# Optimization experiments

Measured on AMD Instinct MI355X. Metric: run time of the kernel, lower is better.

The kernel has to match this reference:

```python
import jax, jax.numpy as jnp
import numpy as np

# ---- static config (from init_kwargs / hard-coded DMlp structure) ----
B, H, W = 8, 56, 56
C = 576              # dim = 9 * n_feat
NF = 64              # n_feat (channels after PixelShuffle(3))
NH = 6               # num_heads
WS = 7               # window_size
N = H * W
IN_F, HID_F, OUT_F = NF * 25, NF * 16, NF * 9  # DMlp fc dims (1600, 1024, 576)

# the hard-coded 7x7 selection mask in DMlp (25 True positions of 49)
_MASK = np.array([
    [1,0,0,1,0,0,1],
    [0,1,0,1,0,1,0],
    [0,0,1,1,1,0,0],
    [1,1,1,1,1,1,1],
    [0,0,1,1,1,0,0],
    [0,1,0,1,0,1,0],
    [1,0,0,1,0,0,1]], dtype=bool)
_OFFS = [(int(i), int(j)) for i, j in np.argwhere(_MASK)]  # row-major, matches masked_select order


def _rel_pos_index(ws):
    coords = np.stack(np.meshgrid(np.arange(ws), np.arange(ws), indexing='ij'))  # (2, ws, ws)
    cf = coords.reshape(2, -1)
    rel = (cf[:, :, None] - cf[:, None, :]).transpose(1, 2, 0).astype(np.int64)
    rel[..., 0] += ws - 1
    rel[..., 1] += ws - 1
    rel[..., 0] *= 2 * ws - 1
    return rel.sum(-1)  # (ws*ws, ws*ws)

REL_IDX = jnp.asarray(_rel_pos_index(WS))


def layernorm(x, w, b, eps=1e-5):
    mu = x.mean(-1, keepdims=True)
    var = ((x - mu) ** 2).mean(-1, keepdims=True)
    return (x - mu) / jnp.sqrt(var + eps) * w + b


def dmlp(x, fc1_w, fc1_b, fc2_w, fc2_b):
    # x: (B, N, C). Patch_UnEmbed(patch_dim=1) == reshape to (B, C, H, W)
    y = x.transpose(0, 2, 1).reshape(B, C, H, W)
    # PixelShuffle(3): (B, C, H, W) -> (B, NF, 3H, 3W)
    y = y.reshape(B, NF, 3, 3, H, W).transpose(0, 1, 4, 2, 5, 3).reshape(B, NF, 3 * H, 3 * W)
    # ReflectionPad2d(2)
    y = jnp.pad(y, ((0, 0), (0, 0), (2, 2), (2, 2)), mode='reflect')
    # unfold(kernel=7, stride=3) + masked_select: gather only the 25 masked kernel offsets
    cols = jnp.stack([y[:, :, di:di + 3 * H:3, dj:dj + 3 * W:3] for di, dj in _OFFS], axis=-1)  # (B, NF, H, W, 25)
    cols = cols.transpose(0, 2, 3, 1, 4).reshape(B, N, IN_F)  # channel-major then kernel pos, like masked_select
    h = jax.nn.gelu(cols @ fc1_w + fc1_b, approximate=False)
    return h @ fc2_w + fc2_b  # (B, N, OUT_F=C)


def reference(x, norm1_w, norm1_b, qkv_w, qkv_b, rpb_table, proj_w, proj_b,
              norm2_w, norm2_b, fc1_w, fc1_b, fc2_w, fc2_b):
    shortcut = x
    y = layernorm(x, norm1_w, norm1_b).reshape(B, H, W, C)
    # window partition (shift_size = 0, no mask)
    nw = H // WS
    yw = y.reshape(B, nw, WS, nw, WS, C).transpose(0, 1, 3, 2, 4, 5).reshape(-1, WS * WS, C)
    # window attention with relative position bias
    qkv = yw @ qkv_w + qkv_b  # (B*nW^2, 49, 3C)
    hd = C // NH
    q, k, v = [t.reshape(-1, WS * WS, NH, hd).transpose(0, 2, 1, 3) for t in jnp.split(qkv, 3, axis=-1)]
    scale = hd ** -0.5
    attn = jnp.einsum('bhid,bhjd->bhij', q * scale, k)
    bias = rpb_table[REL_IDX].transpose(2, 0, 1)  # (NH, 49, 49)
    attn = jax.nn.softmax(attn + bias[None], axis=-1)
    o = jnp.einsum('bhij,bhjd->bhid', attn, v).transpose(0, 2, 1, 3).reshape(-1, WS * WS, C)
    o = o @ proj_w + proj_b
    # window reverse
    o = o.reshape(B, nw, nw, WS, WS, C).transpose(0, 1, 3, 2, 4, 5).reshape(B, N, C)
    x = shortcut + o
    x = x + dmlp(layernorm(x, norm2_w, norm2_b), fc1_w, fc1_b, fc2_w, fc2_b)
    return x


def setup_inputs() -> dict:
    key = jax.random.key(0)
    ks = jax.random.split(key, 16)
    s = 0.02
    return {
        'x': jax.random.normal(ks[0], (B, N, C), jnp.float32),
        'norm1_w': jnp.ones((C,), jnp.float32),
        'norm1_b': jnp.zeros((C,), jnp.float32),
        'qkv_w': jax.random.normal(ks[1], (C, 3 * C), jnp.float32) * s,
        'qkv_b': jnp.zeros((3 * C,), jnp.float32),
        'rpb_table': jax.random.normal(ks[2], ((2 * WS - 1) ** 2, NH), jnp.float32) * s,
        'proj_w': jax.random.normal(ks[3], (C, C), jnp.float32) * s,
        'proj_b': jnp.zeros((C,), jnp.float32),
        'norm2_w': jnp.ones((C,), jnp.float32),
        'norm2_b': jnp.zeros((C,), jnp.float32),
        'fc1_w': jax.random.normal(ks[4], (IN_F, HID_F), jnp.float32) * s,
        'fc1_b': jnp.zeros((HID_F,), jnp.float32),
        'fc2_w': jax.random.normal(ks[5], (HID_F, OUT_F), jnp.float32) * s,
        'fc2_b': jnp.zeros((OUT_F,), jnp.float32),
    }
```

## Files before the change

kernel.cpp:

```cpp
#include <hip/hip_runtime.h>

typedef unsigned short u16;
typedef __bf16 bf16x8 __attribute__((ext_vector_type(8)));
typedef float f32x4 __attribute__((ext_vector_type(4)));

__device__ __forceinline__ float bf2f(u16 u) {
  union { unsigned int i; float f; } v; v.i = ((unsigned int)u) << 16; return v.f;
}
__device__ __forceinline__ u16 f2bf(float f) {
  union { float f; unsigned int i; } v; v.f = f;
  unsigned int i = v.i;
  return (u16)((i + 0x7fffu + ((i >> 16) & 1u)) >> 16);
}
__device__ __forceinline__ float ldf(const float* p) { return *p; }
__device__ __forceinline__ float ldf(const u16* p) { return bf2f(*p); }

__device__ __forceinline__ float gelu_f(float v) {
  float x = fabsf(v) * 0.70710678118654752f;
  float t = __builtin_amdgcn_rcpf(fmaf(0.3275911f, x, 1.0f));
  float poly = t * fmaf(t, fmaf(t, fmaf(t, fmaf(t, 1.061405429f, -1.453152027f),
                                        1.421413741f), -0.284496736f), 0.254829592f);
  float er = fmaf(-poly, __expf(-x * x), 1.0f);
  er = copysignf(er, v);
  return 0.5f * v * (1.0f + er);
}

__device__ __forceinline__ void load_lds16(const u16* g, u16* l) {
  __builtin_amdgcn_global_load_lds(
      (const __attribute__((address_space(1))) unsigned int*)g,
      (__attribute__((address_space(3))) unsigned int*)l, 16, 0, 0);
}

__global__ void transpose_kernel(const float* __restrict__ W, u16* __restrict__ Wt,
                                 int K, int N) {
  int idx = blockIdx.x * 256 + threadIdx.x;
  if (idx >= K * N) return;
  int k = idx / N, n = idx % N;
  Wt[n * K + k] = f2bf(W[idx]);
}

__global__ void transpose_fc1_kernel(const float* __restrict__ W, u16* __restrict__ Wt) {
  int idx = blockIdx.x * 256 + threadIdx.x;
  if (idx >= 1600 * 1024) return;
  int k = idx >> 10, n = idx & 1023;
  int nf = k / 25, p = k - nf * 25;
  Wt[n * 1600 + p * 64 + nf] = f2bf(W[idx]);
}

template <typename T>
__global__ __launch_bounds__(256) void ln_kernel(const T* __restrict__ x,
                                                 const float* __restrict__ w,
                                                 const float* __restrict__ b,
                                                 u16* __restrict__ out) {
  int wave = threadIdx.x >> 6, lane = threadIdx.x & 63;
  long row = (long)blockIdx.x * 4 + wave;
  const T* xr = x + row * 576;
  float v[9];
  float sum = 0.f;
  #pragma unroll
  for (int i = 0; i < 9; ++i) { v[i] = ldf(&xr[lane + i * 64]); sum += v[i]; }
  #pragma unroll
  for (int off = 32; off; off >>= 1) sum += __shfl_xor(sum, off);
  float mean = sum * (1.0f / 576.0f);
  float var = 0.f;
  #pragma unroll
  for (int i = 0; i < 9; ++i) { float d = v[i] - mean; var += d * d; }
  #pragma unroll
  for (int off = 32; off; off >>= 1) var += __shfl_xor(var, off);
  float rstd = rsqrtf(var * (1.0f / 576.0f) + 1e-5f);
  u16* outr = out + row * 576;
  #pragma unroll
  for (int i = 0; i < 9; ++i) {
    int c = lane + i * 64;
    outr[c] = f2bf((v[i] - mean) * rstd * w[c] + b[c]);
  }
}

__global__ __launch_bounds__(256) void ln_ps_kernel(const float* __restrict__ x,
                                                    const float* __restrict__ w,
                                                    const float* __restrict__ b,
                                                    u16* __restrict__ ps) {
  __shared__ u16 sh[4][576];
  int wave = threadIdx.x >> 6, lane = threadIdx.x & 63;
  long row = (long)blockIdx.x * 4 + wave;
  const float* xr = x + row * 576;
  float v[9];
  float sum = 0.f;
  #pragma unroll
  for (int i = 0; i < 9; ++i) { v[i] = xr[lane + i * 64]; sum += v[i]; }
  #pragma unroll
  for (int off = 32; off; off >>= 1) sum += __shfl_xor(sum, off);
  float mean = sum * (1.0f / 576.0f);
  float var = 0.f;
  #pragma unroll
  for (int i = 0; i < 9; ++i) { float d = v[i] - mean; var += d * d; }
  #pragma unroll
  for (int off = 32; off; off >>= 1) var += __shfl_xor(var, off);
  float rstd = rsqrtf(var * (1.0f / 576.0f) + 1e-5f);
  #pragma unroll
  for (int i = 0; i < 9; ++i) {
    int c = lane + i * 64;
    sh[wave][c] = f2bf((v[i] - mean) * rstd * w[c] + b[c]);
  }
  __syncthreads();
  int bb = (int)(row / 3136), ij = (int)(row % 3136);
  int h2 = ij / 56, w2 = ij - h2 * 56;
  #pragma unroll
  for (int a = 0; a < 3; ++a)
    #pragma unroll
    for (int b2 = 0; b2 < 3; ++b2) {
      u16 val = sh[wave][lane * 9 + a * 3 + b2];
      long off = (((long)bb * 168 + 3 * h2 + a) * 168 + (3 * w2 + b2)) * 64 + lane;
      ps[off] = val;
    }
}

__constant__ int c_di[25] = {0,0,0, 1,1,1, 2,2,2, 3,3,3,3,3,3,3, 4,4,4, 5,5,5, 6,6,6};
__constant__ int c_dj[25] = {0,3,6, 1,3,5, 2,3,4, 0,1,2,3,4,5,6, 2,3,4, 1,3,5, 0,3,6};

__global__ __launch_bounds__(256) void attn_kernel(const u16* __restrict__ qkv,
                                                   const float* __restrict__ rpb,
                                                   u16* __restrict__ obuf) {
  int h = blockIdx.y;
  int wi = blockIdx.x;
  int b = wi >> 6, w = wi & 63, wr = w >> 3, wc = w & 7;
  __shared__ __align__(16) u16 Qs[64 * 104];
  __shared__ __align__(16) u16 Ks[64 * 104];
  __shared__ __align__(16) u16 Vt[96 * 72];
  __shared__ __align__(16) u16 Ps[64 * 72];
  int tid = threadIdx.x;
  int lane = tid & 63, wv = tid >> 6;
  int quad = lane >> 4, l15 = lane & 15;
  const float scale = 0.1020620726159658f;

  long base = ((long)b * 3136 + wr * 7 * 56 + wc * 7) * 1728 + h * 96;

  for (int idx = tid; idx < 588; idx += 256) {
    int t = idx / 12, dq = idx % 12;
    int tr = t / 7, tc = t - tr * 7;
    long roff = base + (tr * 56 + tc) * 1728 + dq * 8;
    *(uint4*)&Qs[t * 104 + dq * 8] = *(const uint4*)(qkv + roff);
    *(uint4*)&Ks[t * 104 + dq * 8] = *(const uint4*)(qkv + roff + 576);
  }
  for (int idx = tid; idx < 96 * 15; idx += 256) {
    int d = idx / 15, t = 49 + idx % 15;
    Vt[d * 72 + t] = 0;
  }
  for (int idx = tid; idx < 768; idx += 256) {
    int dq = idx >> 6, t = idx & 63;
    if (t < 49) {
      int tr = t / 7, tc = t - tr * 7;
      uint4 v = *(const uint4*)(qkv + base + (tr * 56 + tc) * 1728 + 1152 + dq * 8);
      const u16* vv = (const u16*)&v;
      #pragma unroll
      for (int kk = 0; kk < 8; ++kk) Vt[(dq * 8 + kk) * 72 + t] = vv[kk];
    }
  }
  __syncthreads();

  f32x4 accS[4] = {};
  #pragma unroll
  for (int k0 = 0; k0 < 3; ++k0) {
    bf16x8 aq = *(const bf16x8*)&Qs[(wv * 16 + l15) * 104 + k0 * 32 + quad * 8];
    #pragma unroll
    for (int nt = 0; nt < 4; ++nt) {
      bf16x8 bk = *(const bf16x8*)&Ks[(nt * 16 + l15) * 104 + k0 * 32 + quad * 8];
      accS[nt] = __builtin_amdgcn_mfma_f32_16x16x32_bf16(aq, bk, accS[nt], 0, 0, 0);
    }
  }

  #pragma unroll
  for (int r = 0; r < 4; ++r) {
    int rg = wv * 16 + quad * 4 + r;
    int yi = rg / 7, xi = rg - yi * 7;
    float sv[4];
    float mx = -3e38f;
    #pragma unroll
    for (int nt = 0; nt < 4; ++nt) {
      int col = nt * 16 + l15;
      float s = accS[nt][r] * scale;
      if (rg < 49 && col < 49) {
        int yj = col / 7, xj = col - yj * 7;
        s += rpb[((yi - yj + 6) * 13 + (xi - xj + 6)) * 6 + h];
      } else {
        s = -3e38f;
      }
      sv[nt] = s;
      mx = fmaxf(mx, s);
    }
    #pragma unroll
    for (int off = 8; off; off >>= 1) mx = fmaxf(mx, __shfl_xor(mx, off));
    float sum = 0.f;
    #pragma unroll
    for (int nt = 0; nt < 4; ++nt) { sv[nt] = __expf(sv[nt] - mx); sum += sv[nt]; }
    #pragma unroll
    for (int off = 8; off; off >>= 1) sum += __shfl_xor(sum, off);
    float inv = 1.0f / sum;
    u16* psr = Ps + rg * 72;
    #pragma unroll
    for (int nt = 0; nt < 4; ++nt) psr[nt * 16 + l15] = f2bf(sv[nt] * inv);
  }
  __syncthreads();

  f32x4 accO[6] = {};
  #pragma unroll
  for (int k0 = 0; k0 < 2; ++k0) {
    bf16x8 ap = *(const bf16x8*)&Ps[(wv * 16 + l15) * 72 + k0 * 32 + quad * 8];
    #pragma unroll
    for (int nt = 0; nt < 6; ++nt) {
      bf16x8 bv = *(const bf16x8*)&Vt[(nt * 16 + l15) * 72 + k0 * 32 + quad * 8];
      accO[nt] = __builtin_amdgcn_mfma_f32_16x16x32_bf16(ap, bv, accO[nt], 0, 0, 0);
    }
  }
  #pragma unroll
  for (int r = 0; r < 4; ++r) {
    int rg = wv * 16 + quad * 4 + r;
    if (rg < 49) {
      int tr = rg / 7, tc = rg - tr * 7;
      long ooff = ((long)b * 3136 + (wr * 7 + tr) * 56 + wc * 7 + tc) * 576 + h * 96;
      #pragma unroll
      for (int nt = 0; nt < 6; ++nt) obuf[ooff + nt * 16 + l15] = f2bf(accO[nt][r]);
    }
  }
}

template <int EPI, typename TR, typename TO>
__global__ __launch_bounds__(256) void gemm_kernel(const u16* __restrict__ A,
                                                   const u16* __restrict__ Bt,
                                                   const float* __restrict__ bias,
                                                   const TR* __restrict__ res,
                                                   TO* __restrict__ C,
                                                   int M, int N, int K) {
  __shared__ __align__(16) u16 As[3][128 * 32];
  __shared__ __align__(16) u16 Bs[3][128 * 32];

  int nwg = gridDim.x * gridDim.y;
  int flat = blockIdx.y * gridDim.x + blockIdx.x;
  int q = nwg >> 3, r = nwg & 7;
  int xcd = flat & 7, loc = flat >> 3;
  int newflat = ((xcd < r) ? xcd * (q + 1) : r * (q + 1) + (xcd - r) * q) + loc;
  int nblk = newflat % gridDim.x, mblk = newflat / gridDim.x;
  int n0 = nblk * 128;
  int m0 = mblk * 128;

  int tid = threadIdx.x;
  int lane = tid & 63, wv = tid >> 6;
  int quad = lane >> 4, l15 = lane & 15;
  int wr2 = wv >> 1, wc2 = wv & 1;
  f32x4 acc[4][4] = {};

  int rA0 = tid >> 2, rA1 = 64 + (tid >> 2);
  int kc0 = (tid & 3) * 8;
  int rB0 = n0 + rA0; if (rB0 > N - 1) rB0 = N - 1;
  int rB1 = n0 + rA1; if (rB1 > N - 1) rB1 = N - 1;
  const u16* gA0 = A + (long)(m0 + rA0) * K + kc0;
  const u16* gA1 = A + (long)(m0 + rA1) * K + kc0;
  const u16* gB0 = Bt + (long)rB0 * K + kc0;
  const u16* gB1 = Bt + (long)rB1 * K + kc0;
  int lo0 = (wv * 64) * 8, lo1 = (256 + wv * 64) * 8;

  int nt = K >> 5;
  auto stage = [&](int bufi, int kk) {
    load_lds16(gA0 + kk, &As[bufi][lo0]);
    load_lds16(gA1 + kk, &As[bufi][lo1]);
    load_lds16(gB0 + kk, &Bs[bufi][lo0]);
    load_lds16(gB1 + kk, &Bs[bufi][lo1]);
  };
  auto compute = [&](int cur) {
    bf16x8 a[4], bfr[4];
    const u16* as = &As[cur][(wr2 * 64 + l15) * 32 + quad * 8];
    const u16* bs = &Bs[cur][(wc2 * 64 + l15) * 32 + quad * 8];
    #pragma unroll
    for (int mi = 0; mi < 4; ++mi) a[mi] = *(const bf16x8*)(as + mi * 512);
    #pragma unroll
    for (int ni = 0; ni < 4; ++ni) bfr[ni] = *(const bf16x8*)(bs + ni * 512);
    #pragma unroll
    for (int mi = 0; mi < 4; ++mi)
      #pragma unroll
      for (int ni = 0; ni < 4; ++ni)
        acc[mi][ni] = __builtin_amdgcn_mfma_f32_16x16x32_bf16(a[mi], bfr[ni], acc[mi][ni], 0, 0, 0);
  };

  stage(0, 0);
  stage(1, 32);
  int cur = 0, nx2 = 2;
  for (int t = 0; t < nt; ++t) {
    if (t + 2 < nt) {
      stage(nx2, (t + 2) * 32);
      asm volatile("s_waitcnt vmcnt(8)" ::: "memory");
    } else if (t + 1 < nt) {
      asm volatile("s_waitcnt vmcnt(4)" ::: "memory");
    } else {
      asm volatile("s_waitcnt vmcnt(0)" ::: "memory");
    }
    __builtin_amdgcn_s_barrier();
    compute(cur);
    __builtin_amdgcn_s_barrier();
    cur = cur + 1; if (cur == 3) cur = 0;
    nx2 = nx2 + 1; if (nx2 == 3) nx2 = 0;
  }

  #pragma unroll
  for (int mi = 0; mi < 4; ++mi)
    #pragma unroll
    for (int ni = 0; ni < 4; ++ni) {
      int col = n0 + wc2 * 64 + ni * 16 + l15;
      if (col < N) {
        float bz = bias[col];
        #pragma unroll
        for (int rr = 0; rr < 4; ++rr) {
          int row = m0 + wr2 * 64 + mi * 16 + quad * 4 + rr;
          float v = acc[mi][ni][rr] + bz;
          if (EPI == 1) v = gelu_f(v);
          if (EPI == 2) v += ldf(&res[(long)row * N + col]);
          long off = (long)row * N + col;
          if (sizeof(TO) == 2) ((u16*)C)[off] = f2bf(v);
          else                 ((float*)C)[off] = v;
        }
      }
    }
}

__global__ __launch_bounds__(256) void fc1_kernel(const u16* __restrict__ ps,
                                                  const u16* __restrict__ Bt,
                                                  const float* __restrict__ bias,
                                                  u16* __restrict__ C) {
  const int N = 1024, K = 1600;
  __shared__ __align__(16) u16 As[2][128 * 32];
  __shared__ __align__(16) u16 Bs[2][128 * 32];
  __shared__ int s_di[25], s_dj[25];
  if (threadIdx.x < 25) {
    s_di[threadIdx.x] = c_di[threadIdx.x];
    s_dj[threadIdx.x] = c_dj[threadIdx.x];
  }

  int nwg = gridDim.x * gridDim.y;
  int flat = blockIdx.y * gridDim.x + blockIdx.x;
  int q = nwg >> 3;
  int xcd = flat & 7, loc = flat >> 3;
  int newflat = xcd * q + loc;
  int nblk = newflat % gridDim.x, mblk = newflat / gridDim.x;
  int n0 = nblk * 128;
  int m0 = mblk * 128;

  int tid = threadIdx.x;
  int lane = tid & 63, wv = tid >> 6;
  int quad = lane >> 4, l15 = lane & 15;
  int wr2 = wv >> 1, wc2 = wv & 1;
  f32x4 acc[4][4] = {};

  int rA0 = tid >> 2, rA1 = 64 + (tid >> 2);
  int kc0 = (tid & 3) * 8;
  int m0_ = m0 + rA0;
  int b0 = m0_ / 3136, ij0 = m0_ % 3136, i0 = ij0 / 56, j0 = ij0 - i0 * 56;
  int m1_ = m0 + rA1;
  int b1 = m1_ / 3136, ij1 = m1_ % 3136, i1 = ij1 / 56, j1 = ij1 - i1 * 56;
  int u0 = 3 * i0 - 2, v0 = 3 * j0 - 2;
  int u1 = 3 * i1 - 2, v1 = 3 * j1 - 2;
  const u16* psb0 = ps + (long)b0 * 1806336 + kc0;
  const u16* psb1 = ps + (long)b1 * 1806336 + kc0;
  const u16* gB0 = Bt + (long)(n0 + rA0) * K + kc0;
  const u16* gB1 = Bt + (long)(n0 + rA1) * K + kc0;
  int lo0 = (wv * 64) * 8, lo1 = (256 + wv * 64) * 8;

  __syncthreads();

  auto stage = [&](int bufi, int t) {
    int p = t >> 1;
    int dip = s_di[p], djp = s_dj[p];
    int nf = (t & 1) << 5;
    int R0 = u0 + dip; R0 = R0 < 0 ? -R0 : R0; R0 = R0 >= 168 ? 334 - R0 : R0;
    int C0 = v0 + djp; C0 = C0 < 0 ? -C0 : C0; C0 = C0 >= 168 ? 334 - C0 : C0;
    int R1 = u1 + dip; R1 = R1 < 0 ? -R1 : R1; R1 = R1 >= 168 ? 334 - R1 : R1;
    int C1 = v1 + djp; C1 = C1 < 0 ? -C1 : C1; C1 = C1 >= 168 ? 334 - C1 : C1;
    load_lds16(psb0 + (((R0 * 168 + C0) << 6) + nf), &As[bufi][lo0]);
    load_lds16(psb1 + (((R1 * 168 + C1) << 6) + nf), &As[bufi][lo1]);
    load_lds16(gB0 + t * 32, &Bs[bufi][lo0]);
    load_lds16(gB1 + t * 32, &Bs[bufi][lo1]);
  };
  auto compute = [&](int cur) {
    bf16x8 a[4], bfr[4];
    const u16* as = &As[cur][(wr2 * 64 + l15) * 32 + quad * 8];
    const u16* bs = &Bs[cur][(wc2 * 64 + l15) * 32 + quad * 8];
    #pragma unroll
    for (int mi = 0; mi < 4; ++mi) a[mi] = *(const bf16x8*)(as + mi * 512);
    #pragma unroll
    for (int ni = 0; ni < 4; ++ni) bfr[ni] = *(const bf16x8*)(bs + ni * 512);
    #pragma unroll
    for (int mi = 0; mi < 4; ++mi)
      #pragma unroll
      for (int ni = 0; ni < 4; ++ni)
        acc[mi][ni] = __builtin_amdgcn_mfma_f32_16x16x32_bf16(a[mi], bfr[ni], acc[mi][ni], 0, 0, 0);
  };

  const int nt = K >> 5;
  stage(0, 0);
  #pragma unroll 2
  for (int t = 0; t < nt - 1; ++t) {
    int cur = t & 1;
    stage(cur ^ 1, t + 1);
    asm volatile("s_waitcnt vmcnt(4)" ::: "memory");
    __builtin_amdgcn_s_barrier();
    compute(cur);
    __builtin_amdgcn_s_barrier();
  }
  asm volatile("s_waitcnt vmcnt(0)" ::: "memory");
  __builtin_amdgcn_s_barrier();
  compute((nt - 1) & 1);

  #pragma unroll
  for (int mi = 0; mi < 4; ++mi)
    #pragma unroll
    for (int ni = 0; ni < 4; ++ni) {
      int col = n0 + wc2 * 64 + ni * 16 + l15;
      float bz = bias[col];
      #pragma unroll
      for (int rr = 0; rr < 4; ++rr) {
        int row = m0 + wr2 * 64 + mi * 16 + quad * 4 + rr;
        C[(long)row * N + col] = f2bf(gelu_f(acc[mi][ni][rr] + bz));
      }
    }
}

extern "C" void kernel_launch(void* const* d_in, const int* in_sizes, int n_in,
                              void* d_out, int out_size, void* d_ws, size_t ws_size,
                              hipStream_t stream) {
  const float* x      = (const float*)d_in[0];
  const float* n1w    = (const float*)d_in[1];
  const float* n1b    = (const float*)d_in[2];
  const float* qkv_w  = (const float*)d_in[3];
  const float* qkv_b  = (const float*)d_in[4];
  const float* rpb    = (const float*)d_in[5];
  const float* proj_w = (const float*)d_in[6];
  const float* proj_b = (const float*)d_in[7];
  const float* n2w    = (const float*)d_in[8];
  const float* n2b    = (const float*)d_in[9];
  const float* fc1_w  = (const float*)d_in[10];
  const float* fc1_b  = (const float*)d_in[11];
  const float* fc2_w  = (const float*)d_in[12];
  const float* fc2_b  = (const float*)d_in[13];

  char* ws = (char*)d_ws;
  u16* wt_qkv  = (u16*)(ws + 0);
  u16* wt_proj = (u16*)(ws + 1990656);
  u16* wt_fc1  = (u16*)(ws + 2654208);
  u16* wt_fc2  = (u16*)(ws + 5931008);
  char* qkvpool = ws + 7110656;
  char* lnpool  = ws + 50462720;
  u16* ln2ps = (u16*)(ws + 7110656);
  u16* hb    = (u16*)(ws + 36012032);
  float* x1 = (float*)d_out;

  transpose_kernel<<<3888, 256, 0, stream>>>(qkv_w, wt_qkv, 576, 1728);
  transpose_kernel<<<1296, 256, 0, stream>>>(proj_w, wt_proj, 576, 576);
  transpose_fc1_kernel<<<6400, 256, 0, stream>>>(fc1_w, wt_fc1);
  transpose_kernel<<<2304, 256, 0, stream>>>(fc2_w, wt_fc2, 1024, 576);

  for (int h = 0; h < 2; ++h) {
    const long r0 = (long)h * 12544;
    u16* lnb  = (u16*)lnpool;
    u16* qkvb = (u16*)qkvpool;
    ln_kernel<float><<<3136, 256, 0, stream>>>(x + r0 * 576, n1w, n1b, lnb);
    gemm_kernel<0, float, u16><<<dim3(14, 98), 256, 0, stream>>>(
        lnb, wt_qkv, qkv_b, (const float*)nullptr, qkvb, 12544, 1728, 576);
    attn_kernel<<<dim3(256, 6), 256, 0, stream>>>(qkvb, rpb, lnb);
    gemm_kernel<2, float, float><<<dim3(5, 98), 256, 0, stream>>>(
        lnb, wt_proj, proj_b, x + r0 * 576, x1 + r0 * 576, 12544, 576, 576);
  }

  ln_ps_kernel<<<6272, 256, 0, stream>>>(x1, n2w, n2b, ln2ps);
  fc1_kernel<<<dim3(8, 196), 256, 0, stream>>>(ln2ps, wt_fc1, fc1_b, hb);
  gemm_kernel<2, float, float><<<dim3(5, 196), 256, 0, stream>>>(
      hb, wt_fc2, fc2_b, x1, x1, 25088, 576, 1024);
}
```

Before: 534.5 us.

## Widen GEMM K-tile to 64 with XOR-swizzled LDS layout, double buffering

Both the generic GEMM and the fused-unfold fc1 kernel now stage a 64-wide K slice per iteration instead of 32. Each 16-byte chunk is placed in LDS with an XOR swizzle so fragment reads avoid bank conflicts. The generic GEMM drops from triple to double buffering. The change aims to halve the barrier and loop overhead per MFMA and cut LDS conflicts, and in fc1 one K-tile now covers a whole kernel offset (all 64 channels). The cost is more LDS per block (64 KB), which may lower occupancy, and shallower prefetch in the generic GEMM.

```diff
diff --git a/kernel.cpp b/kernel.cpp
--- a/kernel.cpp
+++ b/kernel.cpp
@@ -231,8 +231,8 @@
                                                    const TR* __restrict__ res,
                                                    TO* __restrict__ C,
                                                    int M, int N, int K) {
-  __shared__ __align__(16) u16 As[3][128 * 32];
-  __shared__ __align__(16) u16 Bs[3][128 * 32];
+  __shared__ __align__(16) u16 As[2][128 * 64];
+  __shared__ __align__(16) u16 Bs[2][128 * 64];
 
   int nwg = gridDim.x * gridDim.y;
   int flat = blockIdx.y * gridDim.x + blockIdx.x;
@@ -249,56 +249,55 @@
   int wr2 = wv >> 1, wc2 = wv & 1;
   f32x4 acc[4][4] = {};
 
-  int rA0 = tid >> 2, rA1 = 64 + (tid >> 2);
-  int kc0 = (tid & 3) * 8;
-  int rB0 = n0 + rA0; if (rB0 > N - 1) rB0 = N - 1;
-  int rB1 = n0 + rA1; if (rB1 > N - 1) rB1 = N - 1;
-  const u16* gA0 = A + (long)(m0 + rA0) * K + kc0;
-  const u16* gA1 = A + (long)(m0 + rA1) * K + kc0;
-  const u16* gB0 = Bt + (long)rB0 * K + kc0;
-  const u16* gB1 = Bt + (long)rB1 * K + kc0;
-  int lo0 = (wv * 64) * 8, lo1 = (256 + wv * 64) * 8;
-
-  int nt = K >> 5;
-  auto stage = [&](int bufi, int kk) {
-    load_lds16(gA0 + kk, &As[bufi][lo0]);
-    load_lds16(gA1 + kk, &As[bufi][lo1]);
-    load_lds16(gB0 + kk, &Bs[bufi][lo0]);
-    load_lds16(gB1 + kk, &Bs[bufi][lo1]);
+  int swz = ((tid & 7) ^ ((tid >> 3) & 7)) * 8;
+  int r0 = tid >> 3;
+  const u16 *gAc[4], *gBc[4];
+  #pragma unroll
+  for (int c = 0; c < 4; ++c) {
+    gAc[c] = A + (long)(m0 + c * 32 + r0) * K + swz;
+    int rB = n0 + c * 32 + r0; if (rB > N - 1) rB = N - 1;
+    gBc[c] = Bt + (long)rB * K + swz;
+  }
+  int ldsoff = wv * 512;
+
+  int nt = K >> 6;
+  auto stage = [&](int bufi, int t) {
+    #pragma unroll
+    for (int c = 0; c < 4; ++c) load_lds16(gAc[c] + t * 64, &As[bufi][c * 2048 + ldsoff]);
+    #pragma unroll
+    for (int c = 0; c < 4; ++c) load_lds16(gBc[c] + t * 64, &Bs[bufi][c * 2048 + ldsoff]);
   };
   auto compute = [&](int cur) {
-    bf16x8 a[4], bfr[4];
-    const u16* as = &As[cur][(wr2 * 64 + l15) * 32 + quad * 8];
-    const u16* bs = &Bs[cur][(wc2 * 64 + l15) * 32 + quad * 8];
-    #pragma unroll
-    for (int mi = 0; mi < 4; ++mi) a[mi] = *(const bf16x8*)(as + mi * 512);
-    #pragma unroll
-    for (int ni = 0; ni < 4; ++ni) bfr[ni] = *(const bf16x8*)(bs + ni * 512);
-    #pragma unroll
-    for (int mi = 0; mi < 4; ++mi)
+    #pragma unroll
+    for (int ks = 0; ks < 2; ++ks) {
+      int cc = ((ks * 4 + quad) ^ (l15 & 7)) * 8;
+      bf16x8 a[4], bb[4];
+      #pragma unroll
+      for (int mi = 0; mi < 4; ++mi)
+        a[mi] = *(const bf16x8*)&As[cur][(wr2 * 64 + mi * 16 + l15) * 64 + cc];
       #pragma unroll
       for (int ni = 0; ni < 4; ++ni)
-        acc[mi][ni] = __builtin_amdgcn_mfma_f32_16x16x32_bf16(a[mi], bfr[ni], acc[mi][ni], 0, 0, 0);
+        bb[ni] = *(const bf16x8*)&Bs[cur][(wc2 * 64 + ni * 16 + l15) * 64 + cc];
+      #pragma unroll
+      for (int mi = 0; mi < 4; ++mi)
+        #pragma unroll
+        for (int ni = 0; ni < 4; ++ni)
+          acc[mi][ni] = __builtin_amdgcn_mfma_f32_16x16x32_bf16(a[mi], bb[ni], acc[mi][ni], 0, 0, 0);
+    }
   };
 
   stage(0, 0);
-  stage(1, 32);
-  int cur = 0, nx2 = 2;
-  for (int t = 0; t < nt; ++t) {
-    if (t + 2 < nt) {
-      stage(nx2, (t + 2) * 32);
-      asm volatile("s_waitcnt vmcnt(8)" ::: "memory");
-    } else if (t + 1 < nt) {
-      asm volatile("s_waitcnt vmcnt(4)" ::: "memory");
-    } else {
-      asm volatile("s_waitcnt vmcnt(0)" ::: "memory");
-    }
+  for (int t = 0; t < nt - 1; ++t) {
+    int cur = t & 1;
+    stage(cur ^ 1, t + 1);
+    asm volatile("s_waitcnt vmcnt(8)" ::: "memory");
     __builtin_amdgcn_s_barrier();
     compute(cur);
     __builtin_amdgcn_s_barrier();
-    cur = cur + 1; if (cur == 3) cur = 0;
-    nx2 = nx2 + 1; if (nx2 == 3) nx2 = 0;
-  }
+  }
+  asm volatile("s_waitcnt vmcnt(0)" ::: "memory");
+  __builtin_amdgcn_s_barrier();
+  compute((nt - 1) & 1);
 
   #pragma unroll
   for (int mi = 0; mi < 4; ++mi)
@@ -326,8 +325,8 @@
                                                   const float* __restrict__ bias,
                                                   u16* __restrict__ C) {
   const int N = 1024, K = 1600;
-  __shared__ __align__(16) u16 As[2][128 * 32];
-  __shared__ __align__(16) u16 Bs[2][128 * 32];
+  __shared__ __align__(16) u16 As[2][128 * 64];
+  __shared__ __align__(16) u16 Bs[2][128 * 64];
   __shared__ int s_di[25], s_dj[25];
   if (threadIdx.x < 25) {
     s_di[threadIdx.x] = c_di[threadIdx.x];
@@ -349,57 +348,58 @@
   int wr2 = wv >> 1, wc2 = wv & 1;
   f32x4 acc[4][4] = {};
 
-  int rA0 = tid >> 2, rA1 = 64 + (tid >> 2);
-  int kc0 = (tid & 3) * 8;
-  int m0_ = m0 + rA0;
-  int b0 = m0_ / 3136, ij0 = m0_ % 3136, i0 = ij0 / 56, j0 = ij0 - i0 * 56;
-  int m1_ = m0 + rA1;
-  int b1 = m1_ / 3136, ij1 = m1_ % 3136, i1 = ij1 / 56, j1 = ij1 - i1 * 56;
-  int u0 = 3 * i0 - 2, v0 = 3 * j0 - 2;
-  int u1 = 3 * i1 - 2, v1 = 3 * j1 - 2;
-  const u16* psb0 = ps + (long)b0 * 1806336 + kc0;
-  const u16* psb1 = ps + (long)b1 * 1806336 + kc0;
-  const u16* gB0 = Bt + (long)(n0 + rA0) * K + kc0;
-  const u16* gB1 = Bt + (long)(n0 + rA1) * K + kc0;
-  int lo0 = (wv * 64) * 8, lo1 = (256 + wv * 64) * 8;
+  int swz = ((tid & 7) ^ ((tid >> 3) & 7)) * 8;
+  int r0 = tid >> 3;
+  int uc[4], vc[4];
+  const u16 *psb[4], *gBc[4];
+  #pragma unroll
+  for (int c = 0; c < 4; ++c) {
+    int m_ = m0 + c * 32 + r0;
+    int b_ = m_ / 3136, ij = m_ % 3136, i_ = ij / 56, j_ = ij - i_ * 56;
+    uc[c] = 3 * i_ - 2; vc[c] = 3 * j_ - 2;
+    psb[c] = ps + (long)b_ * 1806336 + swz;
+    gBc[c] = Bt + (long)(n0 + c * 32 + r0) * K + swz;
+  }
+  int ldsoff = wv * 512;
 
   __syncthreads();
 
   auto stage = [&](int bufi, int t) {
-    int p = t >> 1;
-    int dip = s_di[p], djp = s_dj[p];
-    int nf = (t & 1) << 5;
-    int R0 = u0 + dip; R0 = R0 < 0 ? -R0 : R0; R0 = R0 >= 168 ? 334 - R0 : R0;
-    int C0 = v0 + djp; C0 = C0 < 0 ? -C0 : C0; C0 = C0 >= 168 ? 334 - C0 : C0;
-    int R1 = u1 + dip; R1 = R1 < 0 ? -R1 : R1; R1 = R1 >= 168 ? 334 - R1 : R1;
-    int C1 = v1 + djp; C1 = C1 < 0 ? -C1 : C1; C1 = C1 >= 168 ? 334 - C1 : C1;
-    load_lds16(psb0 + (((R0 * 168 + C0) << 6) + nf), &As[bufi][lo0]);
-    load_lds16(psb1 + (((R1 * 168 + C1) << 6) + nf), &As[bufi][lo1]);
-    load_lds16(gB0 + t * 32, &Bs[bufi][lo0]);
-    load_lds16(gB1 + t * 32, &Bs[bufi][lo1]);
+    int dip = s_di[t], djp = s_dj[t];
+    #pragma unroll
+    for (int c = 0; c < 4; ++c) {
+      int R = uc[c] + dip; R = R < 0 ? -R : R; R = R >= 168 ? 334 - R : R;
+      int Cc = vc[c] + djp; Cc = Cc < 0 ? -Cc : Cc; Cc = Cc >= 168 ? 334 - Cc : Cc;
+      load_lds16(psb[c] + ((R * 168 + Cc) << 6), &As[bufi][c * 2048 + ldsoff]);
+    }
+    #pragma unroll
+    for (int c = 0; c < 4; ++c) load_lds16(gBc[c] + t * 64, &Bs[bufi][c * 2048 + ldsoff]);
   };
   auto compute = [&](int cur) {
-    bf16x8 a[4], bfr[4];
-    const u16* as = &As[cur][(wr2 * 64 + l15) * 32 + quad * 8];
-    const u16* bs = &Bs[cur][(wc2 * 64 + l15) * 32 + quad * 8];
-    #pragma unroll
-    for (int mi = 0; mi < 4; ++mi) a[mi] = *(const bf16x8*)(as + mi * 512);
-    #pragma unroll
-    for (int ni = 0; ni < 4; ++ni) bfr[ni] = *(const bf16x8*)(bs + ni * 512);
-    #pragma unroll
-    for (int mi = 0; mi < 4; ++mi)
+    #pragma unroll
+    for (int ks = 0; ks < 2; ++ks) {
+      int cc = ((ks * 4 + quad) ^ (l15 & 7)) * 8;
+      bf16x8 a[4], bb[4];
+      #pragma unroll
+      for (int mi = 0; mi < 4; ++mi)
+        a[mi] = *(const bf16x8*)&As[cur][(wr2 * 64 + mi * 16 + l15) * 64 + cc];
       #pragma unroll
       for (int ni = 0; ni < 4; ++ni)
-        acc[mi][ni] = __builtin_amdgcn_mfma_f32_16x16x32_bf16(a[mi], bfr[ni], acc[mi][ni], 0, 0, 0);
+        bb[ni] = *(const bf16x8*)&Bs[cur][(wc2 * 64 + ni * 16 + l15) * 64 + cc];
+      #pragma unroll
+      for (int mi = 0; mi < 4; ++mi)
+        #pragma unroll
+        for (int ni = 0; ni < 4; ++ni)
+          acc[mi][ni] = __builtin_amdgcn_mfma_f32_16x16x32_bf16(a[mi], bb[ni], acc[mi][ni], 0, 0, 0);
+    }
   };
 
-  const int nt = K >> 5;
+  const int nt = 25;
   stage(0, 0);
-  #pragma unroll 2
   for (int t = 0; t < nt - 1; ++t) {
     int cur = t & 1;
     stage(cur ^ 1, t + 1);
-    asm volatile("s_waitcnt vmcnt(4)" ::: "memory");
+    asm volatile("s_waitcnt vmcnt(8)" ::: "memory");
     __builtin_amdgcn_s_barrier();
     compute(cur);
     __builtin_amdgcn_s_barrier();
```

Result: slower. 554.2 us (+3.7%).
